# Kernel optimization log

Hardware: AMD Instinct MI355X
Metric: run time of the kernel (lower is better)

## Reference

```python
import jax, jax.numpy as jnp
import numpy as np

K = 2  # binary (k-ary) heap-layout tree: children of node j are K*j+1 .. K*j+K

def _levels(N):
    # level of node i in heap layout = floor(log2(i+1)); returns list of index arrays, root level first
    lev = np.floor(np.log2(np.arange(N) + 1)).astype(np.int64)
    depth = int(lev.max()) + 1
    return [np.where(lev == l)[0] for l in range(depth)]

def setup_inputs() -> dict:
    key = jax.random.key(0)
    ks = jax.random.split(key, 9)
    B, N, D = 512, 127, 300
    s = 0.05
    return {
        'x':     jax.random.normal(ks[0], (B, N, D), jnp.float32),
        'Wioux': jax.random.normal(ks[1], (D, 3 * D), jnp.float32) * s,
        'bioux': jax.random.normal(ks[2], (3 * D,), jnp.float32) * s,
        'Wiouh': jax.random.normal(ks[3], (D, 3 * D), jnp.float32) * s,
        'biouh': jax.random.normal(ks[4], (3 * D,), jnp.float32) * s,
        'Wfx':   jax.random.normal(ks[5], (D, D), jnp.float32) * s,
        'bfx':   jax.random.normal(ks[6], (D,), jnp.float32) * s,
        'Wfh':   jax.random.normal(ks[7], (D, D), jnp.float32) * s,
        'bfh':   jax.random.normal(ks[8], (D,), jnp.float32) * s,
    }

def reference(x, Wioux, bioux, Wiouh, biouh, Wfx, bfx, Wfh, bfh):
    # Child-Sum Tree-LSTM, level-synchronous (leaves -> root), batched over B trees.
    B, N, D = x.shape
    levels = _levels(N)
    H = jnp.zeros((B, N, D), x.dtype)
    C = jnp.zeros((B, N, D), x.dtype)
    for idx in reversed(levels):  # process deepest level first
        ch = idx[:, None] * K + 1 + np.arange(K)          # [n, K] child node ids (static)
        valid = jnp.asarray((ch < N), x.dtype)[None, :, :, None]  # [1,n,K,1]
        chc = np.minimum(ch, N - 1)
        ch_h = H[:, chc] * valid                           # [B,n,K,D]; padded children -> 0 (leaf case)
        ch_c = C[:, chc] * valid
        h_sum = ch_h.sum(axis=2)                           # child-sum of hidden states [B,n,D]
        xj = x[:, idx]                                     # [B,n,D]
        iou = xj @ Wioux + bioux + h_sum @ Wiouh + biouh   # [B,n,3D]
        i_g, o_g, u_g = jnp.split(iou, 3, axis=-1)
        i_g = jax.nn.sigmoid(i_g)
        o_g = jax.nn.sigmoid(o_g)
        u_g = jnp.tanh(u_g)
        fx = (xj @ Wfx + bfx)[:, :, None, :]               # broadcast over children
        f = jax.nn.sigmoid(jnp.einsum('bnkd,de->bnke', ch_h, Wfh) + bfh + fx)
        c = i_g * u_g + (f * ch_c).sum(axis=2)             # fc sum; padded ch_c==0
        h = o_g * jnp.tanh(c)
        H = H.at[:, idx].set(h)
        C = C.at[:, idx].set(c)
    return H  # per-node hidden states (contexts); root hidden = H[:, 0]
```

## Files before the change

kernel.cpp:

```cpp
#include <hip/hip_runtime.h>
#include <math.h>

#define DIM 300
#define NNODE 127
#define KP 320
#define BK 32
#define ASTR 40
#define MATSZ (KP*KP)

typedef __attribute__((ext_vector_type(8)))  short bf16x8;
typedef __attribute__((ext_vector_type(16))) float f32x16;

__device__ __forceinline__ unsigned short f2bf(float f){
    unsigned u = __float_as_uint(f);
    u += 0x7fffu + ((u >> 16) & 1u);
    return (unsigned short)(u >> 16);
}
__device__ __forceinline__ float sigf(float v){ return 1.0f/(1.0f+__expf(-v)); }
__device__ __forceinline__ float tanh_(float v){
    float t = __expf(-2.0f*fabsf(v));
    float r = (1.0f - t)/(1.0f + t);
    return v < 0.0f ? -r : r;
}

__global__ void prep_weights(const float* __restrict__ Wioux,
                             const float* __restrict__ Wiouh,
                             const float* __restrict__ Wfx,
                             const float* __restrict__ Wfh,
                             unsigned short* __restrict__ WT)
{
    int k = threadIdx.x;
    int n = blockIdx.x;
    int m = blockIdx.y;
    float v = 0.f;
    if (k < DIM && n < DIM){
        if (m < 3)       v = Wioux[k*(3*DIM) + m*DIM + n];
        else if (m < 6)  v = Wiouh[k*(3*DIM) + (m-3)*DIM + n];
        else if (m == 6) v = Wfx[k*DIM + n];
        else             v = Wfh[k*DIM + n];
    }
    WT[m*MATSZ + n*KP + k] = f2bf(v);
}

__global__ __launch_bounds__(256,2)
void leaf_mfma(const float* __restrict__ x,
               const float* __restrict__ bioux, const float* __restrict__ biouh,
               const unsigned short* __restrict__ WT,
               float* __restrict__ H, float* __restrict__ C)
{
    __shared__ __attribute__((aligned(16))) short lds[(1+3)*64*ASTR];
    short* As = lds;
    short* Bs = lds + 64*ASTR;

    const int t = threadIdx.x;
    const int lane = t & 63, wave = t >> 6;
    const int wm = wave >> 1, wn = wave & 1;
    const int lrow = lane & 31, half = lane >> 5;
    const int rowBase = blockIdx.x * 64;
    const int d0 = blockIdx.y * 64;

    const int sr = t >> 2, sseg = t & 3;
    const float* xrow;
    {
        int grow = rowBase + sr;
        int b = grow >> 6, j = 63 + (grow & 63);
        xrow = x + (b*NNODE + j)*DIM;
    }
    const int bm = t >> 5, bn = t & 31;

    f32x16 accI, accO, accU;
    #pragma unroll
    for (int i = 0; i < 16; i++){ accI[i]=0.f; accO[i]=0.f; accU[i]=0.f; }

    for (int k0 = 0; k0 < KP; k0 += BK){
        {
            int kk0 = k0 + sseg*8;
            bf16x8 px;
            if (kk0 + 8 <= DIM){
                float4 a0 = *(const float4*)(xrow + kk0);
                float4 a1 = *(const float4*)(xrow + kk0 + 4);
                px[0]=f2bf(a0.x); px[1]=f2bf(a0.y); px[2]=f2bf(a0.z); px[3]=f2bf(a0.w);
                px[4]=f2bf(a1.x); px[5]=f2bf(a1.y); px[6]=f2bf(a1.z); px[7]=f2bf(a1.w);
            } else {
                #pragma unroll
                for (int e = 0; e < 8; e++){
                    int k = kk0 + e;
                    px[e] = f2bf(k < DIM ? xrow[k] : 0.f);
                }
            }
            *(bf16x8*)(As + sr*ASTR + sseg*8) = px;
        }
        if (bm < 3){
            const unsigned short* wb = WT + bm*MATSZ + k0;
            #pragma unroll
            for (int h2 = 0; h2 < 2; h2++){
                int nn = bn + 32*h2;
                const unsigned short* src = wb + (d0 + nn)*KP;
                short* dst = Bs + bm*64*ASTR + nn*ASTR;
                *(bf16x8*)(dst)      = *(const bf16x8*)(src);
                *(bf16x8*)(dst + 8)  = *(const bf16x8*)(src + 8);
                *(bf16x8*)(dst + 16) = *(const bf16x8*)(src + 16);
                *(bf16x8*)(dst + 24) = *(const bf16x8*)(src + 24);
            }
        }
        __syncthreads();
        #pragma unroll
        for (int kk = 0; kk < 2; kk++){
            int ao = (wm*32 + lrow)*ASTR + kk*16 + half*8;
            bf16x8 ax = *(const bf16x8*)(As + ao);
            int bo = (wn*32 + lrow)*ASTR + kk*16 + half*8;
            bf16x8 b0 = *(const bf16x8*)(Bs + 0*64*ASTR + bo);
            bf16x8 b1 = *(const bf16x8*)(Bs + 1*64*ASTR + bo);
            bf16x8 b2 = *(const bf16x8*)(Bs + 2*64*ASTR + bo);
            accI = __builtin_amdgcn_mfma_f32_32x32x16_bf16(ax, b0, accI, 0, 0, 0);
            accO = __builtin_amdgcn_mfma_f32_32x32x16_bf16(ax, b1, accO, 0, 0, 0);
            accU = __builtin_amdgcn_mfma_f32_32x32x16_bf16(ax, b2, accU, 0, 0, 0);
        }
        __syncthreads();
    }
    int d = d0 + wn*32 + lrow;
    if (d < DIM){
        float bi  = bioux[d]       + biouh[d];
        float bo_ = bioux[DIM+d]   + biouh[DIM+d];
        float bu  = bioux[2*DIM+d] + biouh[2*DIM+d];
        #pragma unroll
        for (int q = 0; q < 16; q++){
            int grow = rowBase + wm*32 + (q&3) + 8*(q>>2) + 4*half;
            int b = grow >> 6, j = 63 + (grow & 63);
            int obase = (b*NNODE + j)*DIM + d;
            float iv = sigf (accI[q] + bi);
            float ov = sigf (accO[q] + bo_);
            float uv = tanh_(accU[q] + bu);
            float cv = iv*uv;
            C[obase] = cv;
            H[obase] = ov*tanh_(cv);
        }
    }
}

__global__ __launch_bounds__(256,2)
void level_mfma(const float* __restrict__ x,
                const float* __restrict__ bioux, const float* __restrict__ biouh,
                const float* __restrict__ bfx,   const float* __restrict__ bfh,
                const unsigned short* __restrict__ WT,
                float* __restrict__ H, float* __restrict__ C,
                int lo, int lshift)
{
    __shared__ __attribute__((aligned(16))) short lds[(4+8)*64*ASTR];
    short* As = lds;
    short* Bs = lds + 4*64*ASTR;

    const int t = threadIdx.x;
    const int lane = t & 63, wave = t >> 6;
    const int wm = wave >> 1, wn = wave & 1;
    const int lrow = lane & 31, half = lane >> 5;
    const int rowBase = blockIdx.x * 64;
    const int d0 = blockIdx.y * 64;
    const int nmask = (1 << lshift) - 1;

    const int sr = t >> 2, sseg = t & 3;
    const float *xrow, *h0row, *h1row;
    {
        int grow = rowBase + sr;
        int b = grow >> lshift, j = lo + (grow & nmask);
        xrow  = x + (b*NNODE + j)*DIM;
        h0row = H + (b*NNODE + 2*j+1)*DIM;
        h1row = H + (b*NNODE + 2*j+2)*DIM;
    }
    const int bm = t >> 5, bn = t & 31;

    f32x16 accI, accO, accU, accFx, accF0, accF1;
    #pragma unroll
    for (int i = 0; i < 16; i++){
        accI[i]=0.f; accO[i]=0.f; accU[i]=0.f;
        accFx[i]=0.f; accF0[i]=0.f; accF1[i]=0.f;
    }

    for (int k0 = 0; k0 < KP; k0 += BK){
        {
            int kk0 = k0 + sseg*8;
            int aoff = sr*ASTR + sseg*8;
            bf16x8 px;
            if (kk0 + 8 <= DIM){
                float4 a0 = *(const float4*)(xrow + kk0);
                float4 a1 = *(const float4*)(xrow + kk0 + 4);
                px[0]=f2bf(a0.x); px[1]=f2bf(a0.y); px[2]=f2bf(a0.z); px[3]=f2bf(a0.w);
                px[4]=f2bf(a1.x); px[5]=f2bf(a1.y); px[6]=f2bf(a1.z); px[7]=f2bf(a1.w);
            } else {
                #pragma unroll
                for (int e = 0; e < 8; e++){
                    int k = kk0 + e;
                    px[e] = f2bf(k < DIM ? xrow[k] : 0.f);
                }
            }
            *(bf16x8*)(As + aoff) = px;

            float h0v[8], h1v[8];
            if (kk0 + 8 <= DIM){
                float4 b0 = *(const float4*)(h0row + kk0);
                float4 b1 = *(const float4*)(h0row + kk0 + 4);
                float4 c0 = *(const float4*)(h1row + kk0);
                float4 c1 = *(const float4*)(h1row + kk0 + 4);
                h0v[0]=b0.x; h0v[1]=b0.y; h0v[2]=b0.z; h0v[3]=b0.w;
                h0v[4]=b1.x; h0v[5]=b1.y; h0v[6]=b1.z; h0v[7]=b1.w;
                h1v[0]=c0.x; h1v[1]=c0.y; h1v[2]=c0.z; h1v[3]=c0.w;
                h1v[4]=c1.x; h1v[5]=c1.y; h1v[6]=c1.z; h1v[7]=c1.w;
            } else {
                #pragma unroll
                for (int e = 0; e < 8; e++){
                    int k = kk0 + e;
                    bool ok = k < DIM;
                    h0v[e] = ok ? h0row[k] : 0.f;
                    h1v[e] = ok ? h1row[k] : 0.f;
                }
            }
            bf16x8 ph, p0, p1;
            #pragma unroll
            for (int e = 0; e < 8; e++){
                p0[e] = f2bf(h0v[e]);
                p1[e] = f2bf(h1v[e]);
                ph[e] = f2bf(h0v[e] + h1v[e]);
            }
            *(bf16x8*)(As + 1*64*ASTR + aoff) = ph;
            *(bf16x8*)(As + 2*64*ASTR + aoff) = p0;
            *(bf16x8*)(As + 3*64*ASTR + aoff) = p1;
        }
        {
            const unsigned short* wb = WT + bm*MATSZ + k0;
            #pragma unroll
            for (int h2 = 0; h2 < 2; h2++){
                int nn = bn + 32*h2;
                const unsigned short* src = wb + (d0 + nn)*KP;
                short* dst = Bs + bm*64*ASTR + nn*ASTR;
                *(bf16x8*)(dst)      = *(const bf16x8*)(src);
                *(bf16x8*)(dst + 8)  = *(const bf16x8*)(src + 8);
                *(bf16x8*)(dst + 16) = *(const bf16x8*)(src + 16);
                *(bf16x8*)(dst + 24) = *(const bf16x8*)(src + 24);
            }
        }
        __syncthreads();
        #pragma unroll
        for (int kk = 0; kk < 2; kk++){
            int ao = (wm*32 + lrow)*ASTR + kk*16 + half*8;
            bf16x8 ax = *(const bf16x8*)(As + 0*64*ASTR + ao);
            bf16x8 ah = *(const bf16x8*)(As + 1*64*ASTR + ao);
            bf16x8 a0 = *(const bf16x8*)(As + 2*64*ASTR + ao);
            bf16x8 a1 = *(const bf16x8*)(As + 3*64*ASTR + ao);
            int bo = (wn*32 + lrow)*ASTR + kk*16 + half*8;
            bf16x8 b0 = *(const bf16x8*)(Bs + 0*64*ASTR + bo);
            bf16x8 b1 = *(const bf16x8*)(Bs + 1*64*ASTR + bo);
            bf16x8 b2 = *(const bf16x8*)(Bs + 2*64*ASTR + bo);
            bf16x8 b3 = *(const bf16x8*)(Bs + 3*64*ASTR + bo);
            bf16x8 b4 = *(const bf16x8*)(Bs + 4*64*ASTR + bo);
            bf16x8 b5 = *(const bf16x8*)(Bs + 5*64*ASTR + bo);
            bf16x8 b6 = *(const bf16x8*)(Bs + 6*64*ASTR + bo);
            bf16x8 b7 = *(const bf16x8*)(Bs + 7*64*ASTR + bo);
            accI  = __builtin_amdgcn_mfma_f32_32x32x16_bf16(ax, b0, accI , 0, 0, 0);
            accI  = __builtin_amdgcn_mfma_f32_32x32x16_bf16(ah, b3, accI , 0, 0, 0);
            accO  = __builtin_amdgcn_mfma_f32_32x32x16_bf16(ax, b1, accO , 0, 0, 0);
            accO  = __builtin_amdgcn_mfma_f32_32x32x16_bf16(ah, b4, accO , 0, 0, 0);
            accU  = __builtin_amdgcn_mfma_f32_32x32x16_bf16(ax, b2, accU , 0, 0, 0);
            accU  = __builtin_amdgcn_mfma_f32_32x32x16_bf16(ah, b5, accU , 0, 0, 0);
            accFx = __builtin_amdgcn_mfma_f32_32x32x16_bf16(ax, b6, accFx, 0, 0, 0);
            accF0 = __builtin_amdgcn_mfma_f32_32x32x16_bf16(a0, b7, accF0, 0, 0, 0);
            accF1 = __builtin_amdgcn_mfma_f32_32x32x16_bf16(a1, b7, accF1, 0, 0, 0);
        }
        __syncthreads();
    }
    int d = d0 + wn*32 + lrow;
    if (d < DIM){
        float bi  = bioux[d]       + biouh[d];
        float bo_ = bioux[DIM+d]   + biouh[DIM+d];
        float bu  = bioux[2*DIM+d] + biouh[2*DIM+d];
        float bf_ = bfx[d] + bfh[d];
        #pragma unroll
        for (int q = 0; q < 16; q++){
            int grow = rowBase + wm*32 + (q&3) + 8*(q>>2) + 4*half;
            int b = grow >> lshift, j = lo + (grow & nmask);
            int obase = (b*NNODE + j)*DIM + d;
            int c0i = (b*NNODE + 2*j+1)*DIM + d;
            int c1i = (b*NNODE + 2*j+2)*DIM + d;
            float iv = sigf (accI[q] + bi);
            float ov = sigf (accO[q] + bo_);
            float uv = tanh_(accU[q] + bu);
            float f0 = sigf (accFx[q] + accF0[q] + bf_);
            float f1 = sigf (accFx[q] + accF1[q] + bf_);
            float cv = iv*uv + f0*C[c0i] + f1*C[c1i];
            C[obase] = cv;
            H[obase] = ov*tanh_(cv);
        }
    }
}

extern "C" void kernel_launch(void* const* d_in, const int* in_sizes, int n_in,
                              void* d_out, int out_size, void* d_ws, size_t ws_size,
                              hipStream_t stream) {
    const float* x     = (const float*)d_in[0];
    const float* Wioux = (const float*)d_in[1];
    const float* bioux = (const float*)d_in[2];
    const float* Wiouh = (const float*)d_in[3];
    const float* biouh = (const float*)d_in[4];
    const float* Wfx   = (const float*)d_in[5];
    const float* bfx   = (const float*)d_in[6];
    const float* Wfh   = (const float*)d_in[7];
    const float* bfh   = (const float*)d_in[8];
    float* H = (float*)d_out;
    float* C = (float*)d_ws;
    unsigned short* WT = (unsigned short*)((char*)d_ws + 78028800);

    prep_weights<<<dim3(KP, 8), KP, 0, stream>>>(Wioux, Wiouh, Wfx, Wfh, WT);
    leaf_mfma<<<dim3(512, 5), 256, 0, stream>>>(x, bioux, biouh, WT, H, C);
    for (int l = 5; l >= 0; l--){
        level_mfma<<<dim3(8 << l, 5), 256, 0, stream>>>(
            x, bioux, biouh, bfx, bfh, WT, H, C, (1 << l) - 1, l);
    }
}
```

Measured before the change: 533.8 us.

## Use 128-row tiles, direct global-to-LDS weight loads, and XOR-swizzled LDS

Doubles the row tile per block to 128 rows with two MFMA row-tiles per wave, so each weight tile loaded into LDS is reused twice. Weight tiles move into LDS with global_load_lds, and the LDS layout drops padding in favour of an XOR swizzle meant to avoid bank conflicts. The level kernel no longer builds an h_sum or separate Fx operand; it runs extra MFMAs on each child's h directly, adding MFMA work in exchange for less conversion work and staging. Register use and LDS size grow, which may lower occupancy, and the grid halves.

```diff
diff --git a/kernel.cpp b/kernel.cpp
--- a/kernel.cpp
+++ b/kernel.cpp
@@ -2,14 +2,12 @@
 #include <math.h>
 
 #define DIM 300
-#define NNODE 127
+#define NN 127
 #define KP 320
-#define BK 32
-#define ASTR 40
 #define MATSZ (KP*KP)
 
-typedef __attribute__((ext_vector_type(8)))  short bf16x8;
-typedef __attribute__((ext_vector_type(16))) float f32x16;
+typedef short bf16x8 __attribute__((ext_vector_type(8)));
+typedef float f32x16 __attribute__((ext_vector_type(16)));
 
 __device__ __forceinline__ unsigned short f2bf(float f){
     unsigned u = __float_as_uint(f);
@@ -22,6 +20,13 @@
     float r = (1.0f - t)/(1.0f + t);
     return v < 0.0f ? -r : r;
 }
+__device__ __forceinline__ void glds16(const void* g, void* l){
+    __builtin_amdgcn_global_load_lds(
+        (const __attribute__((address_space(1))) unsigned int*)g,
+        (__attribute__((address_space(3))) unsigned int*)l, 16, 0, 0);
+}
+
+#define MFMA __builtin_amdgcn_mfma_f32_32x32x16_bf16
 
 __global__ void prep_weights(const float* __restrict__ Wioux,
                              const float* __restrict__ Wiouh,
@@ -48,73 +53,85 @@
                const unsigned short* __restrict__ WT,
                float* __restrict__ H, float* __restrict__ C)
 {
-    __shared__ __attribute__((aligned(16))) short lds[(1+3)*64*ASTR];
-    short* As = lds;
-    short* Bs = lds + 64*ASTR;
-
-    const int t = threadIdx.x;
-    const int lane = t & 63, wave = t >> 6;
+    __shared__ __attribute__((aligned(16))) short lds[10240];
+    const int t = threadIdx.x, lane = t & 63, wave = t >> 6;
     const int wm = wave >> 1, wn = wave & 1;
     const int lrow = lane & 31, half = lane >> 5;
-    const int rowBase = blockIdx.x * 64;
-    const int d0 = blockIdx.y * 64;
-
-    const int sr = t >> 2, sseg = t & 3;
-    const float* xrow;
-    {
-        int grow = rowBase + sr;
+    const int rowBase = blockIdx.x * 128, d0 = blockIdx.y * 64;
+
+    const float* aptr[2]; int adst[2]; int acg[2];
+    #pragma unroll
+    for (int i = 0; i < 2; i++){
+        int ca = wave*2 + i;
+        int r = ca*16 + (lane >> 2);
+        int grow = rowBase + r;
         int b = grow >> 6, j = 63 + (grow & 63);
-        xrow = x + (b*NNODE + j)*DIM;
-    }
-    const int bm = t >> 5, bn = t & 31;
-
-    f32x16 accI, accO, accU;
-    #pragma unroll
-    for (int i = 0; i < 16; i++){ accI[i]=0.f; accO[i]=0.f; accU[i]=0.f; }
-
-    for (int k0 = 0; k0 < KP; k0 += BK){
-        {
-            int kk0 = k0 + sseg*8;
-            bf16x8 px;
-            if (kk0 + 8 <= DIM){
-                float4 a0 = *(const float4*)(xrow + kk0);
-                float4 a1 = *(const float4*)(xrow + kk0 + 4);
-                px[0]=f2bf(a0.x); px[1]=f2bf(a0.y); px[2]=f2bf(a0.z); px[3]=f2bf(a0.w);
-                px[4]=f2bf(a1.x); px[5]=f2bf(a1.y); px[6]=f2bf(a1.z); px[7]=f2bf(a1.w);
+        int cg = (lane & 3) ^ (r & 3);
+        aptr[i] = x + (b*NN + j)*DIM + cg*8;
+        acg[i] = cg;
+        adst[i] = ca*512 + lane*8;
+    }
+    const unsigned short* bptr[3]; short* bdst[3];
+    #pragma unroll
+    for (int i = 0; i < 3; i++){
+        int cb = wave*3 + i;
+        int m = cb >> 2, g = cb & 3;
+        int n = g*16 + (lane >> 2);
+        int cg = (lane & 3) ^ (n & 3);
+        bptr[i] = WT + m*MATSZ + (d0 + n)*KP + cg*8;
+        bdst[i] = lds + 4096 + cb*512;
+    }
+
+    f32x16 accI[2], accO[2], accU[2];
+    #pragma unroll
+    for (int rt = 0; rt < 2; rt++)
+        #pragma unroll
+        for (int q = 0; q < 16; q++){ accI[rt][q]=0.f; accO[rt][q]=0.f; accU[rt][q]=0.f; }
+
+    #pragma unroll
+    for (int ks = 0; ks < 10; ks++){
+        #pragma unroll
+        for (int i = 0; i < 3; i++) glds16(bptr[i] + ks*32, bdst[i]);
+        #pragma unroll
+        for (int i = 0; i < 2; i++){
+            bf16x8 v;
+            if ((ks+1)*32 <= DIM){
+                float4 p0 = *(const float4*)(aptr[i] + ks*32);
+                float4 p1 = *(const float4*)(aptr[i] + ks*32 + 4);
+                v[0]=f2bf(p0.x); v[1]=f2bf(p0.y); v[2]=f2bf(p0.z); v[3]=f2bf(p0.w);
+                v[4]=f2bf(p1.x); v[5]=f2bf(p1.y); v[6]=f2bf(p1.z); v[7]=f2bf(p1.w);
             } else {
+                int kc = ks*32 + acg[i]*8;
                 #pragma unroll
-                for (int e = 0; e < 8; e++){
-                    int k = kk0 + e;
-                    px[e] = f2bf(k < DIM ? xrow[k] : 0.f);
+                for (int e = 0; e < 8; e++) v[e] = 0;
+                if (kc + 8 <= DIM){
+                    float4 p0 = *(const float4*)(aptr[i] + ks*32);
+                    float4 p1 = *(const float4*)(aptr[i] + ks*32 + 4);
+                    v[0]=f2bf(p0.x); v[1]=f2bf(p0.y); v[2]=f2bf(p0.z); v[3]=f2bf(p0.w);
+                    v[4]=f2bf(p1.x); v[5]=f2bf(p1.y); v[6]=f2bf(p1.z); v[7]=f2bf(p1.w);
+                } else if (kc < DIM){
+                    float4 p0 = *(const float4*)(aptr[i] + ks*32);
+                    v[0]=f2bf(p0.x); v[1]=f2bf(p0.y); v[2]=f2bf(p0.z); v[3]=f2bf(p0.w);
                 }
             }
-            *(bf16x8*)(As + sr*ASTR + sseg*8) = px;
-        }
-        if (bm < 3){
-            const unsigned short* wb = WT + bm*MATSZ + k0;
+            *(bf16x8*)(lds + adst[i]) = v;
+        }
+        __syncthreads();
+        #pragma unroll
+        for (int kk = 0; kk < 2; kk++){
+            int p = ((kk<<1) + half) ^ (lrow & 3);
+            const short* Bb = lds + 4096 + (wn*32 + lrow)*32 + p*8;
+            bf16x8 b0 = *(const bf16x8*)(Bb);
+            bf16x8 b1 = *(const bf16x8*)(Bb + 2048);
+            bf16x8 b2 = *(const bf16x8*)(Bb + 4096);
+            const short* Ab = lds + (wm*64 + lrow)*32 + p*8;
             #pragma unroll
-            for (int h2 = 0; h2 < 2; h2++){
-                int nn = bn + 32*h2;
-                const unsigned short* src = wb + (d0 + nn)*KP;
-                short* dst = Bs + bm*64*ASTR + nn*ASTR;
-                *(bf16x8*)(dst)      = *(const bf16x8*)(src);
-                *(bf16x8*)(dst + 8)  = *(const bf16x8*)(src + 8);
-                *(bf16x8*)(dst + 16) = *(const bf16x8*)(src + 16);
-                *(bf16x8*)(dst + 24) = *(const bf16x8*)(src + 24);
-            }
-        }
-        __syncthreads();
-        #pragma unroll
-        for (int kk = 0; kk < 2; kk++){
-            int ao = (wm*32 + lrow)*ASTR + kk*16 + half*8;
-            bf16x8 ax = *(const bf16x8*)(As + ao);
-            int bo = (wn*32 + lrow)*ASTR + kk*16 + half*8;
-            bf16x8 b0 = *(const bf16x8*)(Bs + 0*64*ASTR + bo);
-            bf16x8 b1 = *(const bf16x8*)(Bs + 1*64*ASTR + bo);
-            bf16x8 b2 = *(const bf16x8*)(Bs + 2*64*ASTR + bo);
-            accI = __builtin_amdgcn_mfma_f32_32x32x16_bf16(ax, b0, accI, 0, 0, 0);
-            accO = __builtin_amdgcn_mfma_f32_32x32x16_bf16(ax, b1, accO, 0, 0, 0);
-            accU = __builtin_amdgcn_mfma_f32_32x32x16_bf16(ax, b2, accU, 0, 0, 0);
+            for (int rt = 0; rt < 2; rt++){
+                bf16x8 ax = *(const bf16x8*)(Ab + rt*1024);
+                accI[rt] = MFMA(ax, b0, accI[rt], 0, 0, 0);
+                accO[rt] = MFMA(ax, b1, accO[rt], 0, 0, 0);
+                accU[rt] = MFMA(ax, b2, accU[rt], 0, 0, 0);
+            }
         }
         __syncthreads();
     }
@@ -124,17 +141,19 @@
         float bo_ = bioux[DIM+d]   + biouh[DIM+d];
         float bu  = bioux[2*DIM+d] + biouh[2*DIM+d];
         #pragma unroll
-        for (int q = 0; q < 16; q++){
-            int grow = rowBase + wm*32 + (q&3) + 8*(q>>2) + 4*half;
-            int b = grow >> 6, j = 63 + (grow & 63);
-            int obase = (b*NNODE + j)*DIM + d;
-            float iv = sigf (accI[q] + bi);
-            float ov = sigf (accO[q] + bo_);
-            float uv = tanh_(accU[q] + bu);
-            float cv = iv*uv;
-            C[obase] = cv;
-            H[obase] = ov*tanh_(cv);
-        }
+        for (int rt = 0; rt < 2; rt++)
+            #pragma unroll
+            for (int q = 0; q < 16; q++){
+                int grow = rowBase + wm*64 + rt*32 + (q&3) + 8*(q>>2) + 4*half;
+                int b = grow >> 6, j = 63 + (grow & 63);
+                int ob = (b*NN + j)*DIM + d;
+                float iv = sigf (accI[rt][q] + bi);
+                float ov = sigf (accO[rt][q] + bo_);
+                float uv = tanh_(accU[rt][q] + bu);
+                float cv = iv*uv;
+                C[ob] = cv;
+                H[ob] = ov*tanh_(cv);
+            }
     }
 }
 
@@ -146,124 +165,109 @@
                 float* __restrict__ H, float* __restrict__ C,
                 int lo, int lshift)
 {
-    __shared__ __attribute__((aligned(16))) short lds[(4+8)*64*ASTR];
-    short* As = lds;
-    short* Bs = lds + 4*64*ASTR;
-
-    const int t = threadIdx.x;
-    const int lane = t & 63, wave = t >> 6;
+    __shared__ __attribute__((aligned(16))) short lds[28672];
+    const int t = threadIdx.x, lane = t & 63, wave = t >> 6;
     const int wm = wave >> 1, wn = wave & 1;
     const int lrow = lane & 31, half = lane >> 5;
-    const int rowBase = blockIdx.x * 64;
-    const int d0 = blockIdx.y * 64;
+    const int rowBase = blockIdx.x * 128, d0 = blockIdx.y * 64;
     const int nmask = (1 << lshift) - 1;
 
-    const int sr = t >> 2, sseg = t & 3;
-    const float *xrow, *h0row, *h1row;
-    {
-        int grow = rowBase + sr;
+    const float* aptr[6]; int adst[6]; int acg[6];
+    #pragma unroll
+    for (int i = 0; i < 6; i++){
+        int ca = wave*6 + i;
+        int s = ca >> 3, rg = ca & 7;
+        int r = rg*16 + (lane >> 2);
+        int grow = rowBase + r;
         int b = grow >> lshift, j = lo + (grow & nmask);
-        xrow  = x + (b*NNODE + j)*DIM;
-        h0row = H + (b*NNODE + 2*j+1)*DIM;
-        h1row = H + (b*NNODE + 2*j+2)*DIM;
-    }
-    const int bm = t >> 5, bn = t & 31;
-
-    f32x16 accI, accO, accU, accFx, accF0, accF1;
-    #pragma unroll
-    for (int i = 0; i < 16; i++){
-        accI[i]=0.f; accO[i]=0.f; accU[i]=0.f;
-        accFx[i]=0.f; accF0[i]=0.f; accF1[i]=0.f;
-    }
-
-    for (int k0 = 0; k0 < KP; k0 += BK){
-        {
-            int kk0 = k0 + sseg*8;
-            int aoff = sr*ASTR + sseg*8;
-            bf16x8 px;
-            if (kk0 + 8 <= DIM){
-                float4 a0 = *(const float4*)(xrow + kk0);
-                float4 a1 = *(const float4*)(xrow + kk0 + 4);
-                px[0]=f2bf(a0.x); px[1]=f2bf(a0.y); px[2]=f2bf(a0.z); px[3]=f2bf(a0.w);
-                px[4]=f2bf(a1.x); px[5]=f2bf(a1.y); px[6]=f2bf(a1.z); px[7]=f2bf(a1.w);
+        int node = (s == 0) ? j : ((s == 1) ? 2*j+1 : 2*j+2);
+        const float* base = (s == 0) ? x : H;
+        int cg = (lane & 3) ^ (r & 3);
+        aptr[i] = base + (b*NN + node)*DIM + cg*8;
+        acg[i] = cg;
+        adst[i] = ca*512 + lane*8;
+    }
+    const unsigned short* bptr[8]; short* bdst[8];
+    #pragma unroll
+    for (int i = 0; i < 8; i++){
+        int cb = wave*8 + i;
+        int m = cb >> 2, g = cb & 3;
+        int n = g*16 + (lane >> 2);
+        int cg = (lane & 3) ^ (n & 3);
+        bptr[i] = WT + m*MATSZ + (d0 + n)*KP + cg*8;
+        bdst[i] = lds + 12288 + cb*512;
+    }
+
+    f32x16 accI[2], accO[2], accU[2], accF0[2], accF1[2];
+    #pragma unroll
+    for (int rt = 0; rt < 2; rt++)
+        #pragma unroll
+        for (int q = 0; q < 16; q++){
+            accI[rt][q]=0.f; accO[rt][q]=0.f; accU[rt][q]=0.f;
+            accF0[rt][q]=0.f; accF1[rt][q]=0.f;
+        }
+
+    #pragma unroll
+    for (int ks = 0; ks < 10; ks++){
+        #pragma unroll
+        for (int i = 0; i < 8; i++) glds16(bptr[i] + ks*32, bdst[i]);
+        #pragma unroll
+        for (int i = 0; i < 6; i++){
+            bf16x8 v;
+            if ((ks+1)*32 <= DIM){
+                float4 p0 = *(const float4*)(aptr[i] + ks*32);
+                float4 p1 = *(const float4*)(aptr[i] + ks*32 + 4);
+                v[0]=f2bf(p0.x); v[1]=f2bf(p0.y); v[2]=f2bf(p0.z); v[3]=f2bf(p0.w);
+                v[4]=f2bf(p1.x); v[5]=f2bf(p1.y); v[6]=f2bf(p1.z); v[7]=f2bf(p1.w);
             } else {
+                int kc = ks*32 + acg[i]*8;
                 #pragma unroll
-                for (int e = 0; e < 8; e++){
-                    int k = kk0 + e;
-                    px[e] = f2bf(k < DIM ? xrow[k] : 0.f);
+                for (int e = 0; e < 8; e++) v[e] = 0;
+                if (kc + 8 <= DIM){
+                    float4 p0 = *(const float4*)(aptr[i] + ks*32);
+                    float4 p1 = *(const float4*)(aptr[i] + ks*32 + 4);
+                    v[0]=f2bf(p0.x); v[1]=f2bf(p0.y); v[2]=f2bf(p0.z); v[3]=f2bf(p0.w);
+                    v[4]=f2bf(p1.x); v[5]=f2bf(p1.y); v[6]=f2bf(p1.z); v[7]=f2bf(p1.w);
+                } else if (kc < DIM){
+                    float4 p0 = *(const float4*)(aptr[i] + ks*32);
+                    v[0]=f2bf(p0.x); v[1]=f2bf(p0.y); v[2]=f2bf(p0.z); v[3]=f2bf(p0.w);
                 }
             }
-            *(bf16x8*)(As + aoff) = px;
-
-            float h0v[8], h1v[8];
-            if (kk0 + 8 <= DIM){
-                float4 b0 = *(const float4*)(h0row + kk0);
-                float4 b1 = *(const float4*)(h0row + kk0 + 4);
-                float4 c0 = *(const float4*)(h1row + kk0);
-                float4 c1 = *(const float4*)(h1row + kk0 + 4);
-                h0v[0]=b0.x; h0v[1]=b0.y; h0v[2]=b0.z; h0v[3]=b0.w;
-                h0v[4]=b1.x; h0v[5]=b1.y; h0v[6]=b1.z; h0v[7]=b1.w;
-                h1v[0]=c0.x; h1v[1]=c0.y; h1v[2]=c0.z; h1v[3]=c0.w;
-                h1v[4]=c1.x; h1v[5]=c1.y; h1v[6]=c1.z; h1v[7]=c1.w;
-            } else {
-                #pragma unroll
-                for (int e = 0; e < 8; e++){
-                    int k = kk0 + e;
-                    bool ok = k < DIM;
-                    h0v[e] = ok ? h0row[k] : 0.f;
-                    h1v[e] = ok ? h1row[k] : 0.f;
-                }
-            }
-            bf16x8 ph, p0, p1;
+            *(bf16x8*)(lds + adst[i]) = v;
+        }
+        __syncthreads();
+        #pragma unroll
+        for (int kk = 0; kk < 2; kk++){
+            int p = ((kk<<1) + half) ^ (lrow & 3);
+            const short* Bb = lds + 12288 + (wn*32 + lrow)*32 + p*8;
+            bf16x8 b0 = *(const bf16x8*)(Bb);
+            bf16x8 b1 = *(const bf16x8*)(Bb + 2048);
+            bf16x8 b2 = *(const bf16x8*)(Bb + 2*2048);
+            bf16x8 b3 = *(const bf16x8*)(Bb + 3*2048);
+            bf16x8 b4 = *(const bf16x8*)(Bb + 4*2048);
+            bf16x8 b5 = *(const bf16x8*)(Bb + 5*2048);
+            bf16x8 b6 = *(const bf16x8*)(Bb + 6*2048);
+            bf16x8 b7 = *(const bf16x8*)(Bb + 7*2048);
+            const short* Ab = lds + (wm*64 + lrow)*32 + p*8;
             #pragma unroll
-            for (int e = 0; e < 8; e++){
-                p0[e] = f2bf(h0v[e]);
-                p1[e] = f2bf(h1v[e]);
-                ph[e] = f2bf(h0v[e] + h1v[e]);
-            }
-            *(bf16x8*)(As + 1*64*ASTR + aoff) = ph;
-            *(bf16x8*)(As + 2*64*ASTR + aoff) = p0;
-            *(bf16x8*)(As + 3*64*ASTR + aoff) = p1;
-        }
-        {
-            const unsigned short* wb = WT + bm*MATSZ + k0;
-            #pragma unroll
-            for (int h2 = 0; h2 < 2; h2++){
-                int nn = bn + 32*h2;
-                const unsigned short* src = wb + (d0 + nn)*KP;
-                short* dst = Bs + bm*64*ASTR + nn*ASTR;
-                *(bf16x8*)(dst)      = *(const bf16x8*)(src);
-                *(bf16x8*)(dst + 8)  = *(const bf16x8*)(src + 8);
-                *(bf16x8*)(dst + 16) = *(const bf16x8*)(src + 16);
-                *(bf16x8*)(dst + 24) = *(const bf16x8*)(src + 24);
-            }
-        }
-        __syncthreads();
-        #pragma unroll
-        for (int kk = 0; kk < 2; kk++){
-            int ao = (wm*32 + lrow)*ASTR + kk*16 + half*8;
-            bf16x8 ax = *(const bf16x8*)(As + 0*64*ASTR + ao);
-            bf16x8 ah = *(const bf16x8*)(As + 1*64*ASTR + ao);
-            bf16x8 a0 = *(const bf16x8*)(As + 2*64*ASTR + ao);
-            bf16x8 a1 = *(const bf16x8*)(As + 3*64*ASTR + ao);
-            int bo = (wn*32 + lrow)*ASTR + kk*16 + half*8;
-            bf16x8 b0 = *(const bf16x8*)(Bs + 0*64*ASTR + bo);
-            bf16x8 b1 = *(const bf16x8*)(Bs + 1*64*ASTR + bo);
-            bf16x8 b2 = *(const bf16x8*)(Bs + 2*64*ASTR + bo);
-            bf16x8 b3 = *(const bf16x8*)(Bs + 3*64*ASTR + bo);
-            bf16x8 b4 = *(const bf16x8*)(Bs + 4*64*ASTR + bo);
-            bf16x8 b5 = *(const bf16x8*)(Bs + 5*64*ASTR + bo);
-            bf16x8 b6 = *(const bf16x8*)(Bs + 6*64*ASTR + bo);
-            bf16x8 b7 = *(const bf16x8*)(Bs + 7*64*ASTR + bo);
-            accI  = __builtin_amdgcn_mfma_f32_32x32x16_bf16(ax, b0, accI , 0, 0, 0);
-            accI  = __builtin_amdgcn_mfma_f32_32x32x16_bf16(ah, b3, accI , 0, 0, 0);
-            accO  = __builtin_amdgcn_mfma_f32_32x32x16_bf16(ax, b1, accO , 0, 0, 0);
-            accO  = __builtin_amdgcn_mfma_f32_32x32x16_bf16(ah, b4, accO , 0, 0, 0);
-            accU  = __builtin_amdgcn_mfma_f32_32x32x16_bf16(ax, b2, accU , 0, 0, 0);
-            accU  = __builtin_amdgcn_mfma_f32_32x32x16_bf16(ah, b5, accU , 0, 0, 0);
-            accFx = __builtin_amdgcn_mfma_f32_32x32x16_bf16(ax, b6, accFx, 0, 0, 0);
-            accF0 = __builtin_amdgcn_mfma_f32_32x32x16_bf16(a0, b7, accF0, 0, 0, 0);
-            accF1 = __builtin_amdgcn_mfma_f32_32x32x16_bf16(a1, b7, accF1, 0, 0, 0);
+            for (int rt = 0; rt < 2; rt++){
+                bf16x8 ax = *(const bf16x8*)(Ab + rt*1024);
+                bf16x8 a0 = *(const bf16x8*)(Ab + 4096 + rt*1024);
+                bf16x8 a1 = *(const bf16x8*)(Ab + 8192 + rt*1024);
+                accI[rt]  = MFMA(ax, b0, accI[rt], 0, 0, 0);
+                accI[rt]  = MFMA(a0, b3, accI[rt], 0, 0, 0);
+                accI[rt]  = MFMA(a1, b3, accI[rt], 0, 0, 0);
+                accO[rt]  = MFMA(ax, b1, accO[rt], 0, 0, 0);
+                accO[rt]  = MFMA(a0, b4, accO[rt], 0, 0, 0);
+                accO[rt]  = MFMA(a1, b4, accO[rt], 0, 0, 0);
+                accU[rt]  = MFMA(ax, b2, accU[rt], 0, 0, 0);
+                accU[rt]  = MFMA(a0, b5, accU[rt], 0, 0, 0);
+                accU[rt]  = MFMA(a1, b5, accU[rt], 0, 0, 0);
+                accF0[rt] = MFMA(ax, b6, accF0[rt], 0, 0, 0);
+                accF0[rt] = MFMA(a0, b7, accF0[rt], 0, 0, 0);
+                accF1[rt] = MFMA(ax, b6, accF1[rt], 0, 0, 0);
+                accF1[rt] = MFMA(a1, b7, accF1[rt], 0, 0, 0);
+            }
         }
         __syncthreads();
     }
@@ -274,21 +278,23 @@
         float bu  = bioux[2*DIM+d] + biouh[2*DIM+d];
         float bf_ = bfx[d] + bfh[d];
         #pragma unroll
-        for (int q = 0; q < 16; q++){
-            int grow = rowBase + wm*32 + (q&3) + 8*(q>>2) + 4*half;
-            int b = grow >> lshift, j = lo + (grow & nmask);
-            int obase = (b*NNODE + j)*DIM + d;
-            int c0i = (b*NNODE + 2*j+1)*DIM + d;
-            int c1i = (b*NNODE + 2*j+2)*DIM + d;
-            float iv = sigf (accI[q] + bi);
-            float ov = sigf (accO[q] + bo_);
-            float uv = tanh_(accU[q] + bu);
-            float f0 = sigf (accFx[q] + accF0[q] + bf_);
-            float f1 = sigf (accFx[q] + accF1[q] + bf_);
-            float cv = iv*uv + f0*C[c0i] + f1*C[c1i];
-            C[obase] = cv;
-            H[obase] = ov*tanh_(cv);
-        }
+        for (int rt = 0; rt < 2; rt++)
+            #pragma unroll
+            for (int q = 0; q < 16; q++){
+                int grow = rowBase + wm*64 + rt*32 + (q&3) + 8*(q>>2) + 4*half;
+                int b = grow >> lshift, j = lo + (grow & nmask);
+                int ob  = (b*NN + j)*DIM + d;
+                float c0 = C[(b*NN + 2*j+1)*DIM + d];
+                float c1 = C[(b*NN + 2*j+2)*DIM + d];
+                float iv = sigf (accI[rt][q] + bi);
+                float ov = sigf (accO[rt][q] + bo_);
+                float uv = tanh_(accU[rt][q] + bu);
+                float f0 = sigf (accF0[rt][q] + bf_);
+                float f1 = sigf (accF1[rt][q] + bf_);
+                float cv = iv*uv + f0*c0 + f1*c1;
+                C[ob] = cv;
+                H[ob] = ov*tanh_(cv);
+            }
     }
 }
 
@@ -309,9 +315,9 @@
     unsigned short* WT = (unsigned short*)((char*)d_ws + 78028800);
 
     prep_weights<<<dim3(KP, 8), KP, 0, stream>>>(Wioux, Wiouh, Wfx, Wfh, WT);
-    leaf_mfma<<<dim3(512, 5), 256, 0, stream>>>(x, bioux, biouh, WT, H, C);
+    leaf_mfma<<<dim3(256, 5), 256, 0, stream>>>(x, bioux, biouh, WT, H, C);
     for (int l = 5; l >= 0; l--){
-        level_mfma<<<dim3(8 << l, 5), 256, 0, stream>>>(
+        level_mfma<<<dim3(4 << l, 5), 256, 0, stream>>>(
             x, bioux, biouh, bfx, bfh, WT, H, C, (1 << l) - 1, l);
     }
 }
```

New measurement: 604.1 us. 1.13x slower.
